# Optimization experiments

Measured on AMD Instinct MI355X. Metric: run time of the kernel, lower is better.

## Reference

```python
import jax, jax.numpy as jnp
import numpy as np

B, N = 8192, 200  # batch of patches, fixed 200 points per patch


def setup_inputs() -> dict:
    key = jax.random.key(0)
    k1, = jax.random.split(key, 1)
    network_in = jax.random.normal(k1, (B, N, 13), dtype=jnp.float32)
    # learned parameters per build(): outward_shift init 0.25, a init 1, b init 0
    outward_shift = jnp.full((1,), 0.25, dtype=jnp.float32)
    a = jnp.ones((1,), dtype=jnp.float32)
    b = jnp.zeros((1,), dtype=jnp.float32)
    return {"network_in": network_in, "outward_shift": outward_shift, "a": a, "b": b}


def reference(network_in, outward_shift, a, b):
    w = network_in[:, :, 0:1]          # [B,N,1]
    xyz1 = network_in[:, :, 1:4]
    xyz2 = network_in[:, :, 4:7]       # also orig_xyz2
    norm1 = network_in[:, :, 7:10]
    norm2 = network_in[:, :, 10:13]

    w = jax.nn.relu(a * w + b) + 1e-8  # [B,N,1]

    v1 = xyz1 + norm1 * outward_shift
    v2 = xyz2 + norm2 * outward_shift

    w_sum = jnp.sum(w, axis=1)                       # [B,1]
    v1_ctr = jnp.sum(v1 * w, axis=1) / w_sum         # [B,3]
    v2_ctr = jnp.sum(v2 * w, axis=1) / w_sum         # [B,3]
    v1 = v1 - v1_ctr[:, None, :]
    v2 = v2 - v2_ctr[:, None, :]

    # cov = v2^T diag(w) v1, done without materializing the NxN diagonal
    cov = jnp.einsum('bni,bn,bnj->bij', v2, w[:, :, 0], v1)  # [B,3,3]

    # tf.linalg.svd: cov = u diag(s) v^T  ->  jnp svd: cov = u diag(s) vh, v = vh^T
    u, s, vh = jnp.linalg.svd(cov)
    v = jnp.swapaxes(vh, -1, -2)

    VUt = jnp.einsum('bik,bjk->bij', v, u)           # v @ u^T
    det_VUt = jnp.linalg.det(VUt)                    # [B]
    ones = jnp.ones_like(det_VUt)
    d = jnp.stack([ones, ones, det_VUt], axis=-1)    # [B,3]

    # R = v @ diag([1,1,det]) @ u^T
    R = jnp.einsum('bik,bk,bjk->bij', v, d, u)       # [B,3,3]

    t = v1_ctr - jnp.einsum('bij,bj->bi', R, v2_ctr) # [B,3]
    new_coords = jnp.einsum('bij,bnj->bni', R, xyz2) + t[:, None, :]
    return new_coords
```

## Files before the change

kernel.cpp:

```cpp
#include <hip/hip_runtime.h>
#include <math.h>

#define NPTS 200
#define NCH  13
#define BLK  256
#define FLT_PER_BATCH (NPTS * NCH)
#define F4_PER_BATCH  (FLT_PER_BATCH / 4)

__global__ __launch_bounds__(BLK) void reduce_kernel(
    const float* __restrict__ net_in,
    const float* __restrict__ shift_p,
    const float* __restrict__ a_p,
    const float* __restrict__ b_p,
    float* __restrict__ sums)
{
    __shared__ float s_in[4 * FLT_PER_BATCH];
    __shared__ float s_part[4][16][20];

    const int tid = threadIdx.x;
    const int w   = tid >> 6;
    const int l   = tid & 63;
    const int b   = blockIdx.x * 4 + w;

    const float shift = shift_p[0];
    const float aa    = a_p[0];
    const float bb    = b_p[0];

    {
        const float4* src4 = (const float4*)(net_in + (size_t)b * FLT_PER_BATCH);
        float4* dst4 = (float4*)(s_in + w * FLT_PER_BATCH);
        #pragma unroll
        for (int j = 0; j < 10; ++j) dst4[l + 64 * j] = src4[l + 64 * j];
        if (l < 10) dst4[640 + l] = src4[640 + l];
    }

    float acc[16];
    #pragma unroll
    for (int k = 0; k < 16; ++k) acc[k] = 0.f;

    const float* base = s_in + w * FLT_PER_BATCH;
    #pragma unroll
    for (int j = 0; j < 4; ++j) {
        const int p = l + 64 * j;
        if (p < NPTS) {
            const float* q = base + p * NCH;
            float wt = aa * q[0] + bb;
            wt = fmaxf(wt, 0.f) + 1e-8f;
            float v1x = fmaf(shift, q[7],  q[1]);
            float v1y = fmaf(shift, q[8],  q[2]);
            float v1z = fmaf(shift, q[9],  q[3]);
            float v2x = fmaf(shift, q[10], q[4]);
            float v2y = fmaf(shift, q[11], q[5]);
            float v2z = fmaf(shift, q[12], q[6]);
            float wv2x = wt * v2x, wv2y = wt * v2y, wv2z = wt * v2z;
            acc[0] += wt;
            acc[1] += wt * v1x; acc[2] += wt * v1y; acc[3] += wt * v1z;
            acc[4] += wv2x;     acc[5] += wv2y;     acc[6] += wv2z;
            acc[7]  += wv2x * v1x; acc[8]  += wv2x * v1y; acc[9]  += wv2x * v1z;
            acc[10] += wv2y * v1x; acc[11] += wv2y * v1y; acc[12] += wv2y * v1z;
            acc[13] += wv2z * v1x; acc[14] += wv2z * v1y; acc[15] += wv2z * v1z;
        }
    }

    #pragma unroll
    for (int k = 0; k < 16; ++k) {
        acc[k] += __shfl_down(acc[k], 32, 64);
        acc[k] += __shfl_down(acc[k], 16, 64);
    }

    if (l < 16) {
        float4* pp = (float4*)&s_part[w][l][0];
        pp[0] = make_float4(acc[0],  acc[1],  acc[2],  acc[3]);
        pp[1] = make_float4(acc[4],  acc[5],  acc[6],  acc[7]);
        pp[2] = make_float4(acc[8],  acc[9],  acc[10], acc[11]);
        pp[3] = make_float4(acc[12], acc[13], acc[14], acc[15]);
    }
    if (l < 16) {
        float s = 0.f;
        #pragma unroll
        for (int r = 0; r < 16; ++r) s += s_part[w][r][l];
        sums[(size_t)b * 16 + l] = s;
    }
}

__global__ __launch_bounds__(64) void solve_kernel(
    const float* __restrict__ sums,
    float* __restrict__ Rt,
    int B)
{
    const int b = blockIdx.x * 64 + threadIdx.x;
    if (b >= B) return;

    float f[16];
    #pragma unroll
    for (int k = 0; k < 16; ++k) f[k] = sums[(size_t)b * 16 + k];

    const float W = f[0];
    const float invW = 1.0f / W;
    float v1c[3] = { f[1] * invW, f[2] * invW, f[3] * invW };
    float v2c[3] = { f[4] * invW, f[5] * invW, f[6] * invW };

    float S[3][3];
    #pragma unroll
    for (int i = 0; i < 3; ++i)
        #pragma unroll
        for (int j = 0; j < 3; ++j)
            S[i][j] = f[7 + 3 * i + j] - W * v2c[i] * v1c[j];

    const float Sxx = S[0][0], Sxy = S[0][1], Sxz = S[0][2];
    const float Syx = S[1][0], Syy = S[1][1], Syz = S[1][2];
    const float Szx = S[2][0], Szy = S[2][1], Szz = S[2][2];

    float A[4][4];
    A[0][0] = Sxx + Syy + Szz;
    A[0][1] = Syz - Szy;  A[0][2] = Szx - Sxz;  A[0][3] = Sxy - Syx;
    A[1][1] = Sxx - Syy - Szz;
    A[1][2] = Sxy + Syx;  A[1][3] = Szx + Sxz;
    A[2][2] = -Sxx + Syy - Szz;
    A[2][3] = Syz + Szy;
    A[3][3] = -Sxx - Syy + Szz;
    A[1][0] = A[0][1]; A[2][0] = A[0][2]; A[3][0] = A[0][3];
    A[2][1] = A[1][2]; A[3][1] = A[1][3]; A[3][2] = A[2][3];

    float V[4][4] = {{1,0,0,0},{0,1,0,0},{0,0,1,0},{0,0,0,1}};

    const int prs[6][2] = {{0,1},{0,2},{0,3},{1,2},{1,3},{2,3}};
    for (int sweep = 0; sweep < 6; ++sweep) {
        #pragma unroll
        for (int r = 0; r < 6; ++r) {
            const int p = prs[r][0], q = prs[r][1];
            float apq = A[p][q];
            if (apq != 0.0f) {
                float tau = (A[q][q] - A[p][p]) / (2.0f * apq);
                float t = copysignf(1.0f, tau) /
                          (fabsf(tau) + sqrtf(1.0f + tau * tau));
                float c = rsqrtf(1.0f + t * t);
                float s = t * c;
                #pragma unroll
                for (int k = 0; k < 4; ++k) {
                    float a1 = A[p][k], a2 = A[q][k];
                    A[p][k] = c * a1 - s * a2;
                    A[q][k] = s * a1 + c * a2;
                }
                #pragma unroll
                for (int k = 0; k < 4; ++k) {
                    float a1 = A[k][p], a2 = A[k][q];
                    A[k][p] = c * a1 - s * a2;
                    A[k][q] = s * a1 + c * a2;
                }
                #pragma unroll
                for (int k = 0; k < 4; ++k) {
                    float a1 = V[k][p], a2 = V[k][q];
                    V[k][p] = c * a1 - s * a2;
                    V[k][q] = s * a1 + c * a2;
                }
            }
        }
    }

    int best = 0;
    #pragma unroll
    for (int i = 1; i < 4; ++i) if (A[i][i] > A[best][best]) best = i;
    const float q0 = V[0][best], qx = V[1][best], qy = V[2][best], qz = V[3][best];

    const float R00 = q0*q0 + qx*qx - qy*qy - qz*qz;
    const float R01 = 2.0f * (qx*qy - q0*qz);
    const float R02 = 2.0f * (qx*qz + q0*qy);
    const float R10 = 2.0f * (qx*qy + q0*qz);
    const float R11 = q0*q0 - qx*qx + qy*qy - qz*qz;
    const float R12 = 2.0f * (qy*qz - q0*qx);
    const float R20 = 2.0f * (qx*qz - q0*qy);
    const float R21 = 2.0f * (qy*qz + q0*qx);
    const float R22 = q0*q0 - qx*qx - qy*qy + qz*qz;

    const float t0 = v1c[0] - (R00 * v2c[0] + R01 * v2c[1] + R02 * v2c[2]);
    const float t1 = v1c[1] - (R10 * v2c[0] + R11 * v2c[1] + R12 * v2c[2]);
    const float t2 = v1c[2] - (R20 * v2c[0] + R21 * v2c[1] + R22 * v2c[2]);

    float* o = Rt + (size_t)b * 12;
    o[0] = R00; o[1]  = R01; o[2]  = R02;
    o[3] = R10; o[4]  = R11; o[5]  = R12;
    o[6] = R20; o[7]  = R21; o[8]  = R22;
    o[9] = t0;  o[10] = t1;  o[11] = t2;
}

__global__ __launch_bounds__(BLK) void apply_kernel(
    const float* __restrict__ net_in,
    const float* __restrict__ Rt,
    float* __restrict__ out,
    int total)
{
    const int g = blockIdx.x * BLK + threadIdx.x;
    if (g >= total) return;
    const int b = g / NPTS;
    const int p = g - b * NPTS;

    const float* q = net_in + (size_t)b * FLT_PER_BATCH + p * NCH;
    const float x = q[4], y = q[5], z = q[6];

    const float* r = Rt + (size_t)b * 12;
    const float ox = r[0] * x + r[1] * y + r[2] * z + r[9];
    const float oy = r[3] * x + r[4] * y + r[5] * z + r[10];
    const float oz = r[6] * x + r[7] * y + r[8] * z + r[11];

    float* o = out + (size_t)g * 3;
    o[0] = ox; o[1] = oy; o[2] = oz;
}

extern "C" void kernel_launch(void* const* d_in, const int* in_sizes, int n_in,
                              void* d_out, int out_size, void* d_ws, size_t ws_size,
                              hipStream_t stream) {
    const float* net_in  = (const float*)d_in[0];
    const float* shift_p = (const float*)d_in[1];
    const float* a_p     = (const float*)d_in[2];
    const float* b_p     = (const float*)d_in[3];
    float* out = (float*)d_out;

    const int B = in_sizes[0] / FLT_PER_BATCH;

    float* sums = (float*)d_ws;
    float* Rt   = sums + (size_t)B * 16;

    reduce_kernel<<<B / 4, BLK, 0, stream>>>(net_in, shift_p, a_p, b_p, sums);
    solve_kernel<<<(B + 63) / 64, 64, 0, stream>>>(sums, Rt, B);
    apply_kernel<<<(B * NPTS + BLK - 1) / BLK, BLK, 0, stream>>>(net_in, Rt, out, B * NPTS);
}
```

Before: 165.8 us.

## Fuse reduce, solve and apply into one per-patch kernel

Merges the three kernels into one. Each wavefront reduces its patch, broadcasts the 16 sums by shuffle, runs the quaternion Jacobi solve redundantly in every lane, and applies the transform to xyz2 values kept in registers. This removes two launches, the workspace round trips and the second global read of the input. In exchange every lane repeats the eigen-solve, which raises register pressure, and the output stores are strided per lane.

```diff
diff --git a/kernel.cpp b/kernel.cpp
--- a/kernel.cpp
+++ b/kernel.cpp
@@ -7,12 +7,12 @@
 #define FLT_PER_BATCH (NPTS * NCH)
 #define F4_PER_BATCH  (FLT_PER_BATCH / 4)
 
-__global__ __launch_bounds__(BLK) void reduce_kernel(
+__global__ __launch_bounds__(BLK) void svd_align_fused(
     const float* __restrict__ net_in,
     const float* __restrict__ shift_p,
     const float* __restrict__ a_p,
     const float* __restrict__ b_p,
-    float* __restrict__ sums)
+    float* __restrict__ out)
 {
     __shared__ float s_in[4 * FLT_PER_BATCH];
     __shared__ float s_part[4][16][20];
@@ -38,6 +38,8 @@
     #pragma unroll
     for (int k = 0; k < 16; ++k) acc[k] = 0.f;
 
+    float rx[4], ry[4], rz[4];
+
     const float* base = s_in + w * FLT_PER_BATCH;
     #pragma unroll
     for (int j = 0; j < 4; ++j) {
@@ -46,12 +48,14 @@
             const float* q = base + p * NCH;
             float wt = aa * q[0] + bb;
             wt = fmaxf(wt, 0.f) + 1e-8f;
+            float x2 = q[4], y2 = q[5], z2 = q[6];
+            rx[j] = x2; ry[j] = y2; rz[j] = z2;
             float v1x = fmaf(shift, q[7],  q[1]);
             float v1y = fmaf(shift, q[8],  q[2]);
             float v1z = fmaf(shift, q[9],  q[3]);
-            float v2x = fmaf(shift, q[10], q[4]);
-            float v2y = fmaf(shift, q[11], q[5]);
-            float v2z = fmaf(shift, q[12], q[6]);
+            float v2x = fmaf(shift, q[10], x2);
+            float v2y = fmaf(shift, q[11], y2);
+            float v2z = fmaf(shift, q[12], z2);
             float wv2x = wt * v2x, wv2y = wt * v2y, wv2z = wt * v2z;
             acc[0] += wt;
             acc[1] += wt * v1x; acc[2] += wt * v1y; acc[3] += wt * v1z;
@@ -59,6 +63,8 @@
             acc[7]  += wv2x * v1x; acc[8]  += wv2x * v1y; acc[9]  += wv2x * v1z;
             acc[10] += wv2y * v1x; acc[11] += wv2y * v1y; acc[12] += wv2y * v1z;
             acc[13] += wv2z * v1x; acc[14] += wv2z * v1y; acc[15] += wv2z * v1z;
+        } else {
+            rx[j] = 0.f; ry[j] = 0.f; rz[j] = 0.f;
         }
     }
 
@@ -67,7 +73,6 @@
         acc[k] += __shfl_down(acc[k], 32, 64);
         acc[k] += __shfl_down(acc[k], 16, 64);
     }
-
     if (l < 16) {
         float4* pp = (float4*)&s_part[w][l][0];
         pp[0] = make_float4(acc[0],  acc[1],  acc[2],  acc[3]);
@@ -75,41 +80,30 @@
         pp[2] = make_float4(acc[8],  acc[9],  acc[10], acc[11]);
         pp[3] = make_float4(acc[12], acc[13], acc[14], acc[15]);
     }
-    if (l < 16) {
-        float s = 0.f;
+    float tot = 0.f;
+    {
+        const int lk = (l < 16) ? l : 0;
         #pragma unroll
-        for (int r = 0; r < 16; ++r) s += s_part[w][r][l];
-        sums[(size_t)b * 16 + l] = s;
-    }
-}
-
-__global__ __launch_bounds__(64) void solve_kernel(
-    const float* __restrict__ sums,
-    float* __restrict__ Rt,
-    int B)
-{
-    const int b = blockIdx.x * 64 + threadIdx.x;
-    if (b >= B) return;
-
+        for (int r = 0; r < 16; ++r) tot += s_part[w][r][lk];
+    }
     float f[16];
     #pragma unroll
-    for (int k = 0; k < 16; ++k) f[k] = sums[(size_t)b * 16 + k];
+    for (int k = 0; k < 16; ++k) f[k] = __shfl(tot, k, 64);
 
     const float W = f[0];
     const float invW = 1.0f / W;
-    float v1c[3] = { f[1] * invW, f[2] * invW, f[3] * invW };
-    float v2c[3] = { f[4] * invW, f[5] * invW, f[6] * invW };
-
-    float S[3][3];
-    #pragma unroll
-    for (int i = 0; i < 3; ++i)
-        #pragma unroll
-        for (int j = 0; j < 3; ++j)
-            S[i][j] = f[7 + 3 * i + j] - W * v2c[i] * v1c[j];
-
-    const float Sxx = S[0][0], Sxy = S[0][1], Sxz = S[0][2];
-    const float Syx = S[1][0], Syy = S[1][1], Syz = S[1][2];
-    const float Szx = S[2][0], Szy = S[2][1], Szz = S[2][2];
+    const float v1cx = f[1] * invW, v1cy = f[2] * invW, v1cz = f[3] * invW;
+    const float v2cx = f[4] * invW, v2cy = f[5] * invW, v2cz = f[6] * invW;
+
+    const float Sxx = f[7]  - W * v2cx * v1cx;
+    const float Sxy = f[8]  - W * v2cx * v1cy;
+    const float Sxz = f[9]  - W * v2cx * v1cz;
+    const float Syx = f[10] - W * v2cy * v1cx;
+    const float Syy = f[11] - W * v2cy * v1cy;
+    const float Syz = f[12] - W * v2cy * v1cz;
+    const float Szx = f[13] - W * v2cz * v1cx;
+    const float Szy = f[14] - W * v2cz * v1cy;
+    const float Szz = f[15] - W * v2cz * v1cz;
 
     float A[4][4];
     A[0][0] = Sxx + Syy + Szz;
@@ -173,38 +167,22 @@
     const float R21 = 2.0f * (qy*qz + q0*qx);
     const float R22 = q0*q0 - qx*qx - qy*qy + qz*qz;
 
-    const float t0 = v1c[0] - (R00 * v2c[0] + R01 * v2c[1] + R02 * v2c[2]);
-    const float t1 = v1c[1] - (R10 * v2c[0] + R11 * v2c[1] + R12 * v2c[2]);
-    const float t2 = v1c[2] - (R20 * v2c[0] + R21 * v2c[1] + R22 * v2c[2]);
-
-    float* o = Rt + (size_t)b * 12;
-    o[0] = R00; o[1]  = R01; o[2]  = R02;
-    o[3] = R10; o[4]  = R11; o[5]  = R12;
-    o[6] = R20; o[7]  = R21; o[8]  = R22;
-    o[9] = t0;  o[10] = t1;  o[11] = t2;
-}
-
-__global__ __launch_bounds__(BLK) void apply_kernel(
-    const float* __restrict__ net_in,
-    const float* __restrict__ Rt,
-    float* __restrict__ out,
-    int total)
-{
-    const int g = blockIdx.x * BLK + threadIdx.x;
-    if (g >= total) return;
-    const int b = g / NPTS;
-    const int p = g - b * NPTS;
-
-    const float* q = net_in + (size_t)b * FLT_PER_BATCH + p * NCH;
-    const float x = q[4], y = q[5], z = q[6];
-
-    const float* r = Rt + (size_t)b * 12;
-    const float ox = r[0] * x + r[1] * y + r[2] * z + r[9];
-    const float oy = r[3] * x + r[4] * y + r[5] * z + r[10];
-    const float oz = r[6] * x + r[7] * y + r[8] * z + r[11];
-
-    float* o = out + (size_t)g * 3;
-    o[0] = ox; o[1] = oy; o[2] = oz;
+    const float t0 = v1cx - (R00 * v2cx + R01 * v2cy + R02 * v2cz);
+    const float t1 = v1cy - (R10 * v2cx + R11 * v2cy + R12 * v2cz);
+    const float t2 = v1cz - (R20 * v2cx + R21 * v2cy + R22 * v2cz);
+
+    float* ob = out + (size_t)b * (NPTS * 3);
+    #pragma unroll
+    for (int j = 0; j < 4; ++j) {
+        const int p = l + 64 * j;
+        if (p < NPTS) {
+            const float x = rx[j], y = ry[j], z = rz[j];
+            float* o = ob + p * 3;
+            o[0] = R00 * x + R01 * y + R02 * z + t0;
+            o[1] = R10 * x + R11 * y + R12 * z + t1;
+            o[2] = R20 * x + R21 * y + R22 * z + t2;
+        }
+    }
 }
 
 extern "C" void kernel_launch(void* const* d_in, const int* in_sizes, int n_in,
@@ -218,10 +196,5 @@
 
     const int B = in_sizes[0] / FLT_PER_BATCH;
 
-    float* sums = (float*)d_ws;
-    float* Rt   = sums + (size_t)B * 16;
-
-    reduce_kernel<<<B / 4, BLK, 0, stream>>>(net_in, shift_p, a_p, b_p, sums);
-    solve_kernel<<<(B + 63) / 64, 64, 0, stream>>>(sums, Rt, B);
-    apply_kernel<<<(B * NPTS + BLK - 1) / BLK, BLK, 0, stream>>>(net_in, Rt, out, B * NPTS);
+    svd_align_fused<<<B / 4, BLK, 0, stream>>>(net_in, shift_p, a_p, b_p, out);
 }
```

Result: slower. 216.9 us (+30.8%).

## Drop LDS staging in reduce, vectorize loads, and process four points per thread in apply

Applied to the files above, without the earlier changes.

The reduce kernel no longer stages each 200x13 patch in shared memory. Each thread now reads its point straight from global memory with three unaligned 4-wide vector loads plus one scalar load. The apply kernel now handles four points per thread, loading xyz2 as vectors and writing three float4s of output, which cuts the thread count and widens the stores. The solve kernel moves to 256-thread blocks. Strided 52-byte per-thread global reads may coalesce less well than the previous bulk copy into shared memory, and the reduce's lane guard is now hard-coded for 200 points.

```diff
diff --git a/kernel.cpp b/kernel.cpp
--- a/kernel.cpp
+++ b/kernel.cpp
@@ -5,7 +5,8 @@
 #define NCH  13
 #define BLK  256
 #define FLT_PER_BATCH (NPTS * NCH)
-#define F4_PER_BATCH  (FLT_PER_BATCH / 4)
+
+typedef float f4u __attribute__((ext_vector_type(4), aligned(4)));
 
 __global__ __launch_bounds__(BLK) void reduce_kernel(
     const float* __restrict__ net_in,
@@ -14,7 +15,6 @@
     const float* __restrict__ b_p,
     float* __restrict__ sums)
 {
-    __shared__ float s_in[4 * FLT_PER_BATCH];
     __shared__ float s_part[4][16][20];
 
     const int tid = threadIdx.x;
@@ -26,33 +26,31 @@
     const float aa    = a_p[0];
     const float bb    = b_p[0];
 
-    {
-        const float4* src4 = (const float4*)(net_in + (size_t)b * FLT_PER_BATCH);
-        float4* dst4 = (float4*)(s_in + w * FLT_PER_BATCH);
-        #pragma unroll
-        for (int j = 0; j < 10; ++j) dst4[l + 64 * j] = src4[l + 64 * j];
-        if (l < 10) dst4[640 + l] = src4[640 + l];
-    }
+    const float* base = net_in + (size_t)b * FLT_PER_BATCH;
 
     float acc[16];
     #pragma unroll
     for (int k = 0; k < 16; ++k) acc[k] = 0.f;
 
-    const float* base = s_in + w * FLT_PER_BATCH;
     #pragma unroll
     for (int j = 0; j < 4; ++j) {
         const int p = l + 64 * j;
-        if (p < NPTS) {
+        if (j < 3 || l < 8) {
             const float* q = base + p * NCH;
-            float wt = aa * q[0] + bb;
+            const f4u q0 = *(const f4u*)(q);
+            const f4u q1 = *(const f4u*)(q + 4);
+            const f4u q2 = *(const f4u*)(q + 8);
+            const float qs = q[12];
+
+            float wt = aa * q0.x + bb;
             wt = fmaxf(wt, 0.f) + 1e-8f;
-            float v1x = fmaf(shift, q[7],  q[1]);
-            float v1y = fmaf(shift, q[8],  q[2]);
-            float v1z = fmaf(shift, q[9],  q[3]);
-            float v2x = fmaf(shift, q[10], q[4]);
-            float v2y = fmaf(shift, q[11], q[5]);
-            float v2z = fmaf(shift, q[12], q[6]);
-            float wv2x = wt * v2x, wv2y = wt * v2y, wv2z = wt * v2z;
+            const float v1x = fmaf(shift, q1.w, q0.y);
+            const float v1y = fmaf(shift, q2.x, q0.z);
+            const float v1z = fmaf(shift, q2.y, q0.w);
+            const float v2x = fmaf(shift, q2.z, q1.x);
+            const float v2y = fmaf(shift, q2.w, q1.y);
+            const float v2z = fmaf(shift, qs,   q1.z);
+            const float wv2x = wt * v2x, wv2y = wt * v2y, wv2z = wt * v2z;
             acc[0] += wt;
             acc[1] += wt * v1x; acc[2] += wt * v1y; acc[3] += wt * v1z;
             acc[4] += wv2x;     acc[5] += wv2y;     acc[6] += wv2z;
@@ -83,12 +81,12 @@
     }
 }
 
-__global__ __launch_bounds__(64) void solve_kernel(
+__global__ __launch_bounds__(BLK) void solve_kernel(
     const float* __restrict__ sums,
     float* __restrict__ Rt,
     int B)
 {
-    const int b = blockIdx.x * 64 + threadIdx.x;
+    const int b = blockIdx.x * BLK + threadIdx.x;
     if (b >= B) return;
 
     float f[16];
@@ -192,19 +190,29 @@
 {
     const int g = blockIdx.x * BLK + threadIdx.x;
     if (g >= total) return;
-    const int b = g / NPTS;
-    const int p = g - b * NPTS;
-
-    const float* q = net_in + (size_t)b * FLT_PER_BATCH + p * NCH;
-    const float x = q[4], y = q[5], z = q[6];
+    const int b = g / 50;
+    const int q = g - b * 50;
 
     const float* r = Rt + (size_t)b * 12;
-    const float ox = r[0] * x + r[1] * y + r[2] * z + r[9];
-    const float oy = r[3] * x + r[4] * y + r[5] * z + r[10];
-    const float oz = r[6] * x + r[7] * y + r[8] * z + r[11];
-
-    float* o = out + (size_t)g * 3;
-    o[0] = ox; o[1] = oy; o[2] = oz;
+    const float R00 = r[0], R01 = r[1], R02 = r[2];
+    const float R10 = r[3], R11 = r[4], R12 = r[5];
+    const float R20 = r[6], R21 = r[7], R22 = r[8];
+    const float t0  = r[9], t1  = r[10], t2 = r[11];
+
+    const float* base = net_in + (size_t)b * FLT_PER_BATCH + (q * 4) * NCH;
+    float nx[4], ny[4], nz[4];
+    #pragma unroll
+    for (int i = 0; i < 4; ++i) {
+        const f4u v = *(const f4u*)(base + i * NCH + 4);
+        nx[i] = R00 * v.x + R01 * v.y + R02 * v.z + t0;
+        ny[i] = R10 * v.x + R11 * v.y + R12 * v.z + t1;
+        nz[i] = R20 * v.x + R21 * v.y + R22 * v.z + t2;
+    }
+
+    float4* p = (float4*)(out + (size_t)b * (NPTS * 3)) + q * 3;
+    p[0] = make_float4(nx[0], ny[0], nz[0], nx[1]);
+    p[1] = make_float4(ny[1], nz[1], nx[2], ny[2]);
+    p[2] = make_float4(nz[2], nx[3], ny[3], nz[3]);
 }
 
 extern "C" void kernel_launch(void* const* d_in, const int* in_sizes, int n_in,
@@ -222,6 +230,6 @@
     float* Rt   = sums + (size_t)B * 16;
 
     reduce_kernel<<<B / 4, BLK, 0, stream>>>(net_in, shift_p, a_p, b_p, sums);
-    solve_kernel<<<(B + 63) / 64, 64, 0, stream>>>(sums, Rt, B);
-    apply_kernel<<<(B * NPTS + BLK - 1) / BLK, BLK, 0, stream>>>(net_in, Rt, out, B * NPTS);
-}
+    solve_kernel<<<(B + BLK - 1) / BLK, BLK, 0, stream>>>(sums, Rt, B);
+    apply_kernel<<<(B * 50 + BLK - 1) / BLK, BLK, 0, stream>>>(net_in, Rt, out, B * 50);
+}
```

Result: no change. 165.6 us (-0.1%).
